# Performance work log

Hardware: AMD Instinct MI355X
Metric: run time of the kernel (lower is better)

The kernel has to match this reference:

```python
import jax, jax.numpy as jnp
import numpy as np

N_NODES = 100000
N_EDGES = 1000000
NUM_GRAPHS = 500
EPS = 1e-5


def gcn_conv(x, src, dst, W, b, n_nodes):
    # PyG GCNConv: h = x @ W, symmetric norm with self-loops, aggregate at dst, add bias
    h = x @ W
    deg = jnp.zeros((n_nodes,), h.dtype).at[dst].add(1.0) + 1.0  # in-degree + self-loop
    dis = jax.lax.rsqrt(deg)
    msg = h[src] * (dis[src] * dis[dst])[:, None]               # [E, F] gather
    agg = jnp.zeros_like(h).at[dst].add(msg)                    # scatter-add
    return agg + h * (dis * dis)[:, None] + b                   # self-loop term + bias


def bn_eval(x, g, be, m, v):
    return (x - m) * jax.lax.rsqrt(v + EPS) * g + be


def setup_inputs() -> dict:
    key = jax.random.key(0)
    ks = jax.random.split(key, 8)
    edge_index = jax.random.randint(ks[0], (2, N_EDGES), 0, N_NODES, dtype=jnp.int32)
    batch = jnp.sort(jax.random.randint(ks[1], (N_NODES,), 0, NUM_GRAPHS, dtype=jnp.int32))
    d_in, h1, h2, hc, nc = 64, 64, 32, 16, 2
    return {
        "x": jax.random.normal(ks[2], (N_NODES, d_in), jnp.float32),
        "edge_index": edge_index,
        "batch": batch,
        "W1": jax.random.normal(ks[3], (d_in, h1), jnp.float32) / np.sqrt(d_in),
        "b1": jnp.zeros((h1,), jnp.float32),
        "g1": jnp.ones((h1,), jnp.float32),
        "be1": jnp.zeros((h1,), jnp.float32),
        "m1": jnp.zeros((h1,), jnp.float32),
        "v1": jnp.ones((h1,), jnp.float32),
        "W2": jax.random.normal(ks[4], (h1, h2), jnp.float32) / np.sqrt(h1),
        "b2": jnp.zeros((h2,), jnp.float32),
        "g2": jnp.ones((h2,), jnp.float32),
        "be2": jnp.zeros((h2,), jnp.float32),
        "m2": jnp.zeros((h2,), jnp.float32),
        "v2": jnp.ones((h2,), jnp.float32),
        "Wc1": jax.random.normal(ks[5], (h2, hc), jnp.float32) / np.sqrt(h2),
        "bc1": jnp.zeros((hc,), jnp.float32),
        "Wc2": jax.random.normal(ks[6], (hc, nc), jnp.float32) / np.sqrt(hc),
        "bc2": jnp.zeros((nc,), jnp.float32),
    }


def reference(x, edge_index, batch, W1, b1, g1, be1, m1, v1,
              W2, b2, g2, be2, m2, v2, Wc1, bc1, Wc2, bc2):
    src, dst = edge_index[0], edge_index[1]
    n = x.shape[0]
    # encoder layer 1: GCNConv -> BN(eval) -> ReLU  (dropout off in eval)
    h = jax.nn.relu(bn_eval(gcn_conv(x, src, dst, W1, b1, n), g1, be1, m1, v1))
    # encoder layer 2
    h = jax.nn.relu(bn_eval(gcn_conv(h, src, dst, W2, b2, n), g2, be2, m2, v2))
    # global mean pool over graphs
    sums = jax.ops.segment_sum(h, batch, num_segments=NUM_GRAPHS)
    cnts = jax.ops.segment_sum(jnp.ones((n,), h.dtype), batch, num_segments=NUM_GRAPHS)
    z = sums / jnp.maximum(cnts, 1.0)[:, None]                  # [NUM_GRAPHS, h2]
    # classifier MLP
    return jax.nn.relu(z @ Wc1 + bc1) @ Wc2 + bc2               # [NUM_GRAPHS, num_classes]
```

## Files before the change

### kernel.cpp

```cpp
#include <hip/hip_runtime.h>
#include <hip/hip_bf16.h>


#define CHUNK 4096
#define CAP   4096

typedef float floatx2 __attribute__((ext_vector_type(2)));

__global__ void k_zero_misc(int* __restrict__ bucketCursor, float* __restrict__ sums,
                            int nSums) {
    int i = blockIdx.x * blockDim.x + threadIdx.x;
    if (i < 512) bucketCursor[i] = 0;
    int j = i - 512;
    if (j >= 0 && j < nSums) sums[j] = 0.f;
}

__global__ __launch_bounds__(256) void k_binpairs2(
    const int* __restrict__ src, const int* __restrict__ dst,
    int* __restrict__ bucketCursor, unsigned* __restrict__ pairs, int E) {
    __shared__ int lh[512];
    __shared__ int lbase[512];
    for (int i = threadIdx.x; i < 512; i += 256) lh[i] = 0;
    __syncthreads();
    int base = blockIdx.x * CHUNK;
    for (int i = threadIdx.x; i < CHUNK; i += 256) {
        int e = base + i;
        if (e < E) atomicAdd(&lh[dst[e] >> 8], 1);
    }
    __syncthreads();
    for (int i = threadIdx.x; i < 512; i += 256) {
        int c = lh[i];
        lbase[i] = c ? atomicAdd(&bucketCursor[i], c) : 0;
        lh[i] = 0;
    }
    __syncthreads();
    for (int i = threadIdx.x; i < CHUNK; i += 256) {
        int e = base + i;
        if (e < E) {
            int d = dst[e];
            int b = d >> 8;
            int r = atomicAdd(&lh[b], 1);
            pairs[(size_t)b * CAP + lbase[b] + r] =
                ((unsigned)src[e] << 8) | (unsigned)(d & 255);
        }
    }
}

__global__ __launch_bounds__(256) void k_csr2(
    const unsigned* __restrict__ pairs, const int* __restrict__ bucketCursor,
    int* __restrict__ rowStart, int* __restrict__ rowEnd,
    float* __restrict__ dis, int* __restrict__ perm, int n) {
    __shared__ int cnt[256];
    __shared__ int s[256];
    __shared__ int cur[256];
    int b = blockIdx.x, tid = threadIdx.x;
    int total = bucketCursor[b];
    size_t base = (size_t)b * CAP;
    cnt[tid] = 0;
    __syncthreads();
    for (int i = tid; i < total; i += 256) atomicAdd(&cnt[pairs[base + i] & 255], 1);
    __syncthreads();
    int v = cnt[tid];
    s[tid] = v;
    __syncthreads();
    for (int off = 1; off < 256; off <<= 1) {
        int t = (tid >= off) ? s[tid - off] : 0;
        __syncthreads();
        s[tid] += t;
        __syncthreads();
    }
    int excl = s[tid] - v;
    int node = b * 256 + tid;
    if (node < n) {
        rowStart[node] = (int)base + excl;
        rowEnd[node]   = (int)base + excl + v;
        dis[node] = rsqrtf((float)v + 1.0f);
    }
    cur[tid] = excl;
    __syncthreads();
    for (int i = tid; i < total; i += 256) {
        unsigned pr = pairs[base + i];
        int lo = pr & 255;
        int slot = atomicAdd(&cur[lo], 1);
        perm[base + slot] = (int)(pr >> 8);
    }
}

__global__ __launch_bounds__(256) void k_gemm64(
    const float* __restrict__ x, const float* __restrict__ W,
    const float* __restrict__ dis, unsigned char* __restrict__ hs8, int n) {
    __shared__ float Ws[64 * 64];
    __shared__ float xs[128][65];
    const int tid = threadIdx.x;
    for (int i = tid * 4; i < 4096; i += 1024)
        *(float4*)&Ws[i] = *(const float4*)&W[i];
    const int base = blockIdx.x * 128;
    for (int i = tid; i < 2048; i += 256) {
        int r = i >> 4;
        int k = (i & 15) * 4;
        int row = base + r;
        float4 xv = (row < n) ? *(const float4*)&x[(size_t)row * 64 + k]
                              : make_float4(0.f, 0.f, 0.f, 0.f);
        xs[r][k] = xv.x; xs[r][k + 1] = xv.y; xs[r][k + 2] = xv.z; xs[r][k + 3] = xv.w;
    }
    __syncthreads();
    const int cg = tid & 7;
    const int rg = tid >> 3;
    float acc[4][8] = {};
#pragma unroll 4
    for (int k = 0; k < 64; ++k) {
        float w8[8];
        *(float4*)&w8[0] = *(const float4*)&Ws[k * 64 + cg * 8];
        *(float4*)&w8[4] = *(const float4*)&Ws[k * 64 + cg * 8 + 4];
        float x4[4];
#pragma unroll
        for (int rr = 0; rr < 4; ++rr) x4[rr] = xs[rg * 4 + rr][k];
#pragma unroll
        for (int rr = 0; rr < 4; ++rr)
#pragma unroll
            for (int cc = 0; cc < 8; ++cc)
                acc[rr][cc] = fmaf(x4[rr], w8[cc], acc[rr][cc]);
    }
#pragma unroll
    for (int rr = 0; rr < 4; ++rr) {
        int row = base + rg * 4 + rr;
        if (row >= n) break;
        float d = dis[row];
        int q0 = __builtin_amdgcn_cvt_pk_fp8_f32(acc[rr][0] * d, acc[rr][1] * d, 0, false);
        q0 = __builtin_amdgcn_cvt_pk_fp8_f32(acc[rr][2] * d, acc[rr][3] * d, q0, true);
        int q1 = __builtin_amdgcn_cvt_pk_fp8_f32(acc[rr][4] * d, acc[rr][5] * d, 0, false);
        q1 = __builtin_amdgcn_cvt_pk_fp8_f32(acc[rr][6] * d, acc[rr][7] * d, q1, true);
        uint2 q = {(unsigned)q0, (unsigned)q1};
        *(uint2*)&hs8[(size_t)row * 64 + cg * 8] = q;
    }
}

__device__ __forceinline__ void unpack8(uint2 u, float* a) {
    floatx2 p0 = __builtin_amdgcn_cvt_pk_f32_fp8(u.x, false);
    floatx2 p1 = __builtin_amdgcn_cvt_pk_f32_fp8(u.x, true);
    floatx2 p2 = __builtin_amdgcn_cvt_pk_f32_fp8(u.y, false);
    floatx2 p3 = __builtin_amdgcn_cvt_pk_f32_fp8(u.y, true);
    a[0] = p0[0]; a[1] = p0[1]; a[2] = p1[0]; a[3] = p1[1];
    a[4] = p2[0]; a[5] = p2[1]; a[6] = p3[0]; a[7] = p3[1];
}

__global__ __launch_bounds__(256) void k_g64f8_gemm32(
    const unsigned char* __restrict__ hs8, const int* __restrict__ rowStart,
    const int* __restrict__ rowEnd, const int* __restrict__ perm,
    const float* __restrict__ dis,
    const float* __restrict__ b, const float* __restrict__ g,
    const float* __restrict__ be, const float* __restrict__ m,
    const float* __restrict__ v, const float* __restrict__ W2,
    unsigned char* __restrict__ hs2f8, int n) {
    __shared__ float W2s[64 * 32];
    __shared__ float actS[32][68];
    for (int i = threadIdx.x * 4; i < 2048; i += 1024)
        *(float4*)&W2s[i] = *(const float4*)&W2[i];
    __syncthreads();

    const uint2* hsu = (const uint2*)hs8;
    int c = threadIdx.x & 7;
    int ln = threadIdx.x >> 3;
    int node = (blockIdx.x * 256 + threadIdx.x) >> 3;
    if (node >= n) return;
    int r0 = rowStart[node], r1 = rowEnd[node];
    float d = dis[node];
    float a[8];
    unpack8(hsu[(size_t)node * 8 + c], a);
    int e = r0;
    for (; e + 7 < r1; e += 8) {
        int s0 = perm[e],     s1 = perm[e + 1], s2 = perm[e + 2], s3 = perm[e + 3];
        int s4 = perm[e + 4], s5 = perm[e + 5], s6 = perm[e + 6], s7 = perm[e + 7];
        uint2 u0 = hsu[(size_t)s0 * 8 + c];
        uint2 u1 = hsu[(size_t)s1 * 8 + c];
        uint2 u2 = hsu[(size_t)s2 * 8 + c];
        uint2 u3 = hsu[(size_t)s3 * 8 + c];
        uint2 u4 = hsu[(size_t)s4 * 8 + c];
        uint2 u5 = hsu[(size_t)s5 * 8 + c];
        uint2 u6 = hsu[(size_t)s6 * 8 + c];
        uint2 u7 = hsu[(size_t)s7 * 8 + c];
        float t[8];
#pragma unroll
        for (int j = 0; j < 8; ++j) {
            uint2 u = j == 0 ? u0 : j == 1 ? u1 : j == 2 ? u2 : j == 3 ? u3
                    : j == 4 ? u4 : j == 5 ? u5 : j == 6 ? u6 : u7;
            unpack8(u, t);
#pragma unroll
            for (int q = 0; q < 8; ++q) a[q] += t[q];
        }
    }
    for (; e < r1; ++e) {
        float t[8];
        unpack8(hsu[(size_t)perm[e] * 8 + c], t);
#pragma unroll
        for (int q = 0; q < 8; ++q) a[q] += t[q];
    }
    int f = 8 * c;
    float y[8];
#pragma unroll
    for (int h = 0; h < 2; ++h) {
        float4 gv = *(const float4*)&g[f + 4 * h];
        float4 vv = *(const float4*)&v[f + 4 * h];
        float4 bv = *(const float4*)&b[f + 4 * h];
        float4 mv = *(const float4*)&m[f + 4 * h];
        float4 bev = *(const float4*)&be[f + 4 * h];
        float sc0 = gv.x * rsqrtf(vv.x + 1e-5f), sc1 = gv.y * rsqrtf(vv.y + 1e-5f);
        float sc2 = gv.z * rsqrtf(vv.z + 1e-5f), sc3 = gv.w * rsqrtf(vv.w + 1e-5f);
        float y0 = fmaf(a[4 * h + 0] * d, sc0, (bv.x - mv.x) * sc0 + bev.x);
        float y1 = fmaf(a[4 * h + 1] * d, sc1, (bv.y - mv.y) * sc1 + bev.y);
        float y2 = fmaf(a[4 * h + 2] * d, sc2, (bv.z - mv.z) * sc2 + bev.z);
        float y3 = fmaf(a[4 * h + 3] * d, sc3, (bv.w - mv.w) * sc3 + bev.w);
        y[4 * h + 0] = y0 > 0.f ? y0 : 0.f;
        y[4 * h + 1] = y1 > 0.f ? y1 : 0.f;
        y[4 * h + 2] = y2 > 0.f ? y2 : 0.f;
        y[4 * h + 3] = y3 > 0.f ? y3 : 0.f;
    }
    *(float4*)&actS[ln][f]     = *(float4*)&y[0];
    *(float4*)&actS[ln][f + 4] = *(float4*)&y[4];

    float o0 = 0.f, o1 = 0.f, o2 = 0.f, o3 = 0.f;
#pragma unroll
    for (int k = 0; k < 64; ++k) {
        float av = actS[ln][k];
        float4 w = *(const float4*)&W2s[k * 32 + 4 * c];
        o0 = fmaf(av, w.x, o0);
        o1 = fmaf(av, w.y, o1);
        o2 = fmaf(av, w.z, o2);
        o3 = fmaf(av, w.w, o3);
    }
    int q = __builtin_amdgcn_cvt_pk_fp8_f32(o0 * d, o1 * d, 0, false);
    q = __builtin_amdgcn_cvt_pk_fp8_f32(o2 * d, o3 * d, q, true);
    *(unsigned*)&hs2f8[(size_t)node * 32 + 4 * c] = (unsigned)q;
}

__global__ __launch_bounds__(256) void k_g32f8(
    const unsigned char* __restrict__ hs8, const int* __restrict__ rowStart,
    const int* __restrict__ rowEnd, const int* __restrict__ perm,
    const float* __restrict__ dis,
    const float* __restrict__ b, const float* __restrict__ g,
    const float* __restrict__ be, const float* __restrict__ m,
    const float* __restrict__ v, float* __restrict__ act, int n) {
    const uint2* hsu = (const uint2*)hs8;
    int c = threadIdx.x & 3;
    int node = (blockIdx.x * 256 + threadIdx.x) >> 2;
    if (node >= n) return;
    int r0 = rowStart[node], r1 = rowEnd[node];
    float d = dis[node];
    float a[8];
    unpack8(hsu[(size_t)node * 4 + c], a);
    int e = r0;
    for (; e + 7 < r1; e += 8) {
        int s0 = perm[e],     s1 = perm[e + 1], s2 = perm[e + 2], s3 = perm[e + 3];
        int s4 = perm[e + 4], s5 = perm[e + 5], s6 = perm[e + 6], s7 = perm[e + 7];
        uint2 u0 = hsu[(size_t)s0 * 4 + c];
        uint2 u1 = hsu[(size_t)s1 * 4 + c];
        uint2 u2 = hsu[(size_t)s2 * 4 + c];
        uint2 u3 = hsu[(size_t)s3 * 4 + c];
        uint2 u4 = hsu[(size_t)s4 * 4 + c];
        uint2 u5 = hsu[(size_t)s5 * 4 + c];
        uint2 u6 = hsu[(size_t)s6 * 4 + c];
        uint2 u7 = hsu[(size_t)s7 * 4 + c];
        float t[8];
#pragma unroll
        for (int j = 0; j < 8; ++j) {
            uint2 u = j == 0 ? u0 : j == 1 ? u1 : j == 2 ? u2 : j == 3 ? u3
                    : j == 4 ? u4 : j == 5 ? u5 : j == 6 ? u6 : u7;
            unpack8(u, t);
#pragma unroll
            for (int q = 0; q < 8; ++q) a[q] += t[q];
        }
    }
    for (; e < r1; ++e) {
        float t[8];
        unpack8(hsu[(size_t)perm[e] * 4 + c], t);
#pragma unroll
        for (int q = 0; q < 8; ++q) a[q] += t[q];
    }
    int f = 8 * c;
#pragma unroll
    for (int h = 0; h < 2; ++h) {
        float4 gv = *(const float4*)&g[f + 4 * h];
        float4 vv = *(const float4*)&v[f + 4 * h];
        float4 bv = *(const float4*)&b[f + 4 * h];
        float4 mv = *(const float4*)&m[f + 4 * h];
        float4 bev = *(const float4*)&be[f + 4 * h];
        float sc0 = gv.x * rsqrtf(vv.x + 1e-5f), sc1 = gv.y * rsqrtf(vv.y + 1e-5f);
        float sc2 = gv.z * rsqrtf(vv.z + 1e-5f), sc3 = gv.w * rsqrtf(vv.w + 1e-5f);
        float y0 = fmaf(a[4 * h + 0] * d, sc0, (bv.x - mv.x) * sc0 + bev.x);
        float y1 = fmaf(a[4 * h + 1] * d, sc1, (bv.y - mv.y) * sc1 + bev.y);
        float y2 = fmaf(a[4 * h + 2] * d, sc2, (bv.z - mv.z) * sc2 + bev.z);
        float y3 = fmaf(a[4 * h + 3] * d, sc3, (bv.w - mv.w) * sc3 + bev.w);
        float4 o = {y0 > 0.f ? y0 : 0.f, y1 > 0.f ? y1 : 0.f,
                    y2 > 0.f ? y2 : 0.f, y3 > 0.f ? y3 : 0.f};
        *(float4*)&act[(size_t)node * 32 + f + 4 * h] = o;
    }
}

__global__ __launch_bounds__(256) void k_pool(
    const float* __restrict__ act2, const int* __restrict__ batch,
    float* __restrict__ sums, float* __restrict__ cnt, int n) {
    int f = threadIdx.x & 31;
    int chunk = (blockIdx.x * blockDim.x + threadIdx.x) >> 5;
    int nchunks = (gridDim.x * blockDim.x) >> 5;
    int per = (n + nchunks - 1) / nchunks;
    int i0 = chunk * per;
    int i1 = min(n, i0 + per);
    if (i0 >= n) return;
    float acc = 0.f, c = 0.f;
    int cur = batch[i0];
    for (int i = i0; i < i1; ++i) {
        int bg = batch[i];
        if (bg != cur) {
            atomicAdd(&sums[(size_t)cur * 32 + f], acc);
            if (f == 0) atomicAdd(&cnt[cur], c);
            acc = 0.f; c = 0.f; cur = bg;
        }
        acc += act2[(size_t)i * 32 + f];
        c += 1.f;
    }
    atomicAdd(&sums[(size_t)cur * 32 + f], acc);
    if (f == 0) atomicAdd(&cnt[cur], c);
}

__global__ void k_mlp(const float* __restrict__ sums, const float* __restrict__ cnt,
                      const float* __restrict__ Wc1, const float* __restrict__ bc1,
                      const float* __restrict__ Wc2, const float* __restrict__ bc2,
                      float* __restrict__ out, int G) {
    int g = blockIdx.x * blockDim.x + threadIdx.x;
    if (g >= G) return;
    float c = cnt[g];
    c = c < 1.f ? 1.f : c;
    float inv = 1.f / c;
    float z[32];
#pragma unroll
    for (int j = 0; j < 32; ++j) z[j] = sums[(size_t)g * 32 + j] * inv;
    float o0 = bc2[0], o1 = bc2[1];
#pragma unroll
    for (int k = 0; k < 16; ++k) {
        float t = bc1[k];
#pragma unroll
        for (int j = 0; j < 32; ++j) t = fmaf(z[j], Wc1[j * 16 + k], t);
        t = t > 0.f ? t : 0.f;
        o0 = fmaf(t, Wc2[k * 2 + 0], o0);
        o1 = fmaf(t, Wc2[k * 2 + 1], o1);
    }
    out[g * 2 + 0] = o0;
    out[g * 2 + 1] = o1;
}

extern "C" void kernel_launch(void* const* d_in, const int* in_sizes, int n_in,
                              void* d_out, int out_size, void* d_ws, size_t ws_size,
                              hipStream_t stream) {
    const float* x   = (const float*)d_in[0];
    const int* ei    = (const int*)d_in[1];
    const int* batch = (const int*)d_in[2];
    const float* W1  = (const float*)d_in[3];
    const float* b1  = (const float*)d_in[4];
    const float* g1  = (const float*)d_in[5];
    const float* be1 = (const float*)d_in[6];
    const float* m1  = (const float*)d_in[7];
    const float* v1  = (const float*)d_in[8];
    const float* W2  = (const float*)d_in[9];
    const float* b2  = (const float*)d_in[10];
    const float* g2  = (const float*)d_in[11];
    const float* be2 = (const float*)d_in[12];
    const float* m2  = (const float*)d_in[13];
    const float* v2  = (const float*)d_in[14];
    const float* Wc1 = (const float*)d_in[15];
    const float* bc1 = (const float*)d_in[16];
    const float* Wc2 = (const float*)d_in[17];
    const float* bc2 = (const float*)d_in[18];

    const int n = in_sizes[2];
    const int E = in_sizes[1] / 2;
    const int G = out_size / 2;
    const int* srcI = ei;
    const int* dstI = ei + E;
    const int NB = (n + 255) >> 8;

    char* pw = (char*)d_ws;
    auto alloc = [&](size_t bytes) {
        char* r = pw;
        pw += (bytes + 255) & ~(size_t)255;
        return r;
    };
    float*    dis          = (float*)alloc((size_t)n * 4);
    int*      bucketCursor = (int*)alloc(512 * 4);
    unsigned* pairs        = (unsigned*)alloc((size_t)NB * CAP * 4);
    int*      perm         = (int*)alloc((size_t)NB * CAP * 4);
    int*      rowStart     = (int*)alloc((size_t)n * 4);
    int*      rowEnd       = (int*)alloc((size_t)n * 4);
    unsigned char* hs1f8   = (unsigned char*)alloc((size_t)64 * n);
    unsigned char* hs2f8   = (unsigned char*)alloc((size_t)32 * n);
    float*    act2         = (float*)alloc((size_t)32 * n * 4);
    float*    sums         = (float*)alloc((size_t)32 * G * 4 + (size_t)G * 4);
    float*    cntG         = sums + (size_t)32 * G;

    const int NT = 256;
    const int nbE = (E + CHUNK - 1) / CHUNK;
    const int nSums = G * 33;

    k_zero_misc<<<(512 + nSums + NT - 1) / NT, NT, 0, stream>>>(bucketCursor, sums, nSums);
    k_binpairs2<<<nbE, NT, 0, stream>>>(srcI, dstI, bucketCursor, pairs, E);
    k_csr2<<<NB, NT, 0, stream>>>(pairs, bucketCursor, rowStart, rowEnd, dis, perm, n);

    k_gemm64<<<(n + 127) / 128, NT, 0, stream>>>(x, W1, dis, hs1f8, n);
    k_g64f8_gemm32<<<(n * 8 + NT - 1) / NT, NT, 0, stream>>>(
        hs1f8, rowStart, rowEnd, perm, dis, b1, g1, be1, m1, v1, W2, hs2f8, n);

    k_g32f8<<<(n * 4 + NT - 1) / NT, NT, 0, stream>>>(
        hs2f8, rowStart, rowEnd, perm, dis, b2, g2, be2, m2, v2, act2, n);

    k_pool<<<1024, NT, 0, stream>>>(act2, batch, sums, cntG, n);
    k_mlp<<<(G + NT - 1) / NT, NT, 0, stream>>>(sums, cntG, Wc1, bc1, Wc2, bc2,
                                                (float*)d_out, G);
}
```

Before: 128.0 us.

## Fuse layer-2 aggregation with global mean pooling via shared-memory atomics

Merges the second GCN aggregation kernel with the graph pooling kernel. Each block accumulates its nodes' post-ReLU features into per-graph shared-memory bins and then flushes them to global sums with atomics. This drops the full-size act2 intermediate write/read and one kernel launch. In exchange it adds contended LDS atomics, since most lanes in a block hit the same graph, plus extra global atomics per block.

```diff
diff --git a/kernel.cpp b/kernel.cpp
--- a/kernel.cpp
+++ b/kernel.cpp
@@ -233,93 +233,112 @@
     *(unsigned*)&hs2f8[(size_t)node * 32 + 4 * c] = (unsigned)q;
 }
 
-__global__ __launch_bounds__(256) void k_g32f8(
+__global__ __launch_bounds__(256) void k_g32f8_pool(
     const unsigned char* __restrict__ hs8, const int* __restrict__ rowStart,
     const int* __restrict__ rowEnd, const int* __restrict__ perm,
     const float* __restrict__ dis,
     const float* __restrict__ b, const float* __restrict__ g,
     const float* __restrict__ be, const float* __restrict__ m,
-    const float* __restrict__ v, float* __restrict__ act, int n) {
+    const float* __restrict__ v, const int* __restrict__ batch,
+    float* __restrict__ sums, float* __restrict__ cntG, int n) {
+    __shared__ float lsum[64][32];
+    __shared__ float lcnt[64];
     const uint2* hsu = (const uint2*)hs8;
-    int c = threadIdx.x & 3;
-    int node = (blockIdx.x * 256 + threadIdx.x) >> 2;
-    if (node >= n) return;
-    int r0 = rowStart[node], r1 = rowEnd[node];
-    float d = dis[node];
-    float a[8];
-    unpack8(hsu[(size_t)node * 4 + c], a);
-    int e = r0;
-    for (; e + 7 < r1; e += 8) {
-        int s0 = perm[e],     s1 = perm[e + 1], s2 = perm[e + 2], s3 = perm[e + 3];
-        int s4 = perm[e + 4], s5 = perm[e + 5], s6 = perm[e + 6], s7 = perm[e + 7];
-        uint2 u0 = hsu[(size_t)s0 * 4 + c];
-        uint2 u1 = hsu[(size_t)s1 * 4 + c];
-        uint2 u2 = hsu[(size_t)s2 * 4 + c];
-        uint2 u3 = hsu[(size_t)s3 * 4 + c];
-        uint2 u4 = hsu[(size_t)s4 * 4 + c];
-        uint2 u5 = hsu[(size_t)s5 * 4 + c];
-        uint2 u6 = hsu[(size_t)s6 * 4 + c];
-        uint2 u7 = hsu[(size_t)s7 * 4 + c];
-        float t[8];
-#pragma unroll
-        for (int j = 0; j < 8; ++j) {
-            uint2 u = j == 0 ? u0 : j == 1 ? u1 : j == 2 ? u2 : j == 3 ? u3
-                    : j == 4 ? u4 : j == 5 ? u5 : j == 6 ? u6 : u7;
-            unpack8(u, t);
+    int tid = threadIdx.x;
+    int c = tid & 3;
+    int node = (blockIdx.x * 256 + tid) >> 2;
+    int base = blockIdx.x * 64;
+    bool valid = node < n;
+
+    int lastNode = min(base + 63, n - 1);
+    int g0 = batch[base < n ? base : n - 1];
+    int span = batch[lastNode] - g0 + 1;
+    bool ldsPath = span <= 64;
+
+    if (ldsPath) {
+        for (int i = tid; i < span * 32; i += 256) lsum[i >> 5][i & 31] = 0.f;
+        for (int i = tid; i < span; i += 256) lcnt[i] = 0.f;
+    }
+    __syncthreads();
+
+    float y[8];
+    int f = 8 * c;
+    int bg = 0;
+    if (valid) {
+        int r0 = rowStart[node], r1 = rowEnd[node];
+        float d = dis[node];
+        float a[8];
+        unpack8(hsu[(size_t)node * 4 + c], a);
+        int e = r0;
+        for (; e + 7 < r1; e += 8) {
+            int s0 = perm[e],     s1 = perm[e + 1], s2 = perm[e + 2], s3 = perm[e + 3];
+            int s4 = perm[e + 4], s5 = perm[e + 5], s6 = perm[e + 6], s7 = perm[e + 7];
+            uint2 u0 = hsu[(size_t)s0 * 4 + c];
+            uint2 u1 = hsu[(size_t)s1 * 4 + c];
+            uint2 u2 = hsu[(size_t)s2 * 4 + c];
+            uint2 u3 = hsu[(size_t)s3 * 4 + c];
+            uint2 u4 = hsu[(size_t)s4 * 4 + c];
+            uint2 u5 = hsu[(size_t)s5 * 4 + c];
+            uint2 u6 = hsu[(size_t)s6 * 4 + c];
+            uint2 u7 = hsu[(size_t)s7 * 4 + c];
+            float t[8];
+#pragma unroll
+            for (int j = 0; j < 8; ++j) {
+                uint2 u = j == 0 ? u0 : j == 1 ? u1 : j == 2 ? u2 : j == 3 ? u3
+                        : j == 4 ? u4 : j == 5 ? u5 : j == 6 ? u6 : u7;
+                unpack8(u, t);
+#pragma unroll
+                for (int q = 0; q < 8; ++q) a[q] += t[q];
+            }
+        }
+        for (; e < r1; ++e) {
+            float t[8];
+            unpack8(hsu[(size_t)perm[e] * 4 + c], t);
 #pragma unroll
             for (int q = 0; q < 8; ++q) a[q] += t[q];
         }
-    }
-    for (; e < r1; ++e) {
-        float t[8];
-        unpack8(hsu[(size_t)perm[e] * 4 + c], t);
-#pragma unroll
-        for (int q = 0; q < 8; ++q) a[q] += t[q];
-    }
-    int f = 8 * c;
-#pragma unroll
-    for (int h = 0; h < 2; ++h) {
-        float4 gv = *(const float4*)&g[f + 4 * h];
-        float4 vv = *(const float4*)&v[f + 4 * h];
-        float4 bv = *(const float4*)&b[f + 4 * h];
-        float4 mv = *(const float4*)&m[f + 4 * h];
-        float4 bev = *(const float4*)&be[f + 4 * h];
-        float sc0 = gv.x * rsqrtf(vv.x + 1e-5f), sc1 = gv.y * rsqrtf(vv.y + 1e-5f);
-        float sc2 = gv.z * rsqrtf(vv.z + 1e-5f), sc3 = gv.w * rsqrtf(vv.w + 1e-5f);
-        float y0 = fmaf(a[4 * h + 0] * d, sc0, (bv.x - mv.x) * sc0 + bev.x);
-        float y1 = fmaf(a[4 * h + 1] * d, sc1, (bv.y - mv.y) * sc1 + bev.y);
-        float y2 = fmaf(a[4 * h + 2] * d, sc2, (bv.z - mv.z) * sc2 + bev.z);
-        float y3 = fmaf(a[4 * h + 3] * d, sc3, (bv.w - mv.w) * sc3 + bev.w);
-        float4 o = {y0 > 0.f ? y0 : 0.f, y1 > 0.f ? y1 : 0.f,
-                    y2 > 0.f ? y2 : 0.f, y3 > 0.f ? y3 : 0.f};
-        *(float4*)&act[(size_t)node * 32 + f + 4 * h] = o;
-    }
-}
-
-__global__ __launch_bounds__(256) void k_pool(
-    const float* __restrict__ act2, const int* __restrict__ batch,
-    float* __restrict__ sums, float* __restrict__ cnt, int n) {
-    int f = threadIdx.x & 31;
-    int chunk = (blockIdx.x * blockDim.x + threadIdx.x) >> 5;
-    int nchunks = (gridDim.x * blockDim.x) >> 5;
-    int per = (n + nchunks - 1) / nchunks;
-    int i0 = chunk * per;
-    int i1 = min(n, i0 + per);
-    if (i0 >= n) return;
-    float acc = 0.f, c = 0.f;
-    int cur = batch[i0];
-    for (int i = i0; i < i1; ++i) {
-        int bg = batch[i];
-        if (bg != cur) {
-            atomicAdd(&sums[(size_t)cur * 32 + f], acc);
-            if (f == 0) atomicAdd(&cnt[cur], c);
-            acc = 0.f; c = 0.f; cur = bg;
-        }
-        acc += act2[(size_t)i * 32 + f];
-        c += 1.f;
-    }
-    atomicAdd(&sums[(size_t)cur * 32 + f], acc);
-    if (f == 0) atomicAdd(&cnt[cur], c);
+#pragma unroll
+        for (int h = 0; h < 2; ++h) {
+            float4 gv = *(const float4*)&g[f + 4 * h];
+            float4 vv = *(const float4*)&v[f + 4 * h];
+            float4 bv = *(const float4*)&b[f + 4 * h];
+            float4 mv = *(const float4*)&m[f + 4 * h];
+            float4 bev = *(const float4*)&be[f + 4 * h];
+            float sc0 = gv.x * rsqrtf(vv.x + 1e-5f), sc1 = gv.y * rsqrtf(vv.y + 1e-5f);
+            float sc2 = gv.z * rsqrtf(vv.z + 1e-5f), sc3 = gv.w * rsqrtf(vv.w + 1e-5f);
+            float y0 = fmaf(a[4 * h + 0] * d, sc0, (bv.x - mv.x) * sc0 + bev.x);
+            float y1 = fmaf(a[4 * h + 1] * d, sc1, (bv.y - mv.y) * sc1 + bev.y);
+            float y2 = fmaf(a[4 * h + 2] * d, sc2, (bv.z - mv.z) * sc2 + bev.z);
+            float y3 = fmaf(a[4 * h + 3] * d, sc3, (bv.w - mv.w) * sc3 + bev.w);
+            y[4 * h + 0] = y0 > 0.f ? y0 : 0.f;
+            y[4 * h + 1] = y1 > 0.f ? y1 : 0.f;
+            y[4 * h + 2] = y2 > 0.f ? y2 : 0.f;
+            y[4 * h + 3] = y3 > 0.f ? y3 : 0.f;
+        }
+        bg = batch[node];
+        if (ldsPath) {
+            int gl = bg - g0;
+#pragma unroll
+            for (int j = 0; j < 8; ++j) atomicAdd(&lsum[gl][f + j], y[j]);
+            if (c == 0) atomicAdd(&lcnt[gl], 1.f);
+        } else {
+#pragma unroll
+            for (int j = 0; j < 8; ++j) atomicAdd(&sums[(size_t)bg * 32 + f + j], y[j]);
+            if (c == 0) atomicAdd(&cntG[bg], 1.f);
+        }
+    }
+    __syncthreads();
+    if (ldsPath) {
+        for (int i = tid; i < span * 32; i += 256) {
+            int gs = i >> 5, ff = i & 31;
+            float vl = lsum[gs][ff];
+            if (vl != 0.f) atomicAdd(&sums[(size_t)(g0 + gs) * 32 + ff], vl);
+        }
+        for (int i = tid; i < span; i += 256) {
+            float vl = lcnt[i];
+            if (vl != 0.f) atomicAdd(&cntG[g0 + i], vl);
+        }
+    }
 }
 
 __global__ void k_mlp(const float* __restrict__ sums, const float* __restrict__ cnt,
@@ -392,7 +411,6 @@
     int*      rowEnd       = (int*)alloc((size_t)n * 4);
     unsigned char* hs1f8   = (unsigned char*)alloc((size_t)64 * n);
     unsigned char* hs2f8   = (unsigned char*)alloc((size_t)32 * n);
-    float*    act2         = (float*)alloc((size_t)32 * n * 4);
     float*    sums         = (float*)alloc((size_t)32 * G * 4 + (size_t)G * 4);
     float*    cntG         = sums + (size_t)32 * G;
 
@@ -408,10 +426,10 @@
     k_g64f8_gemm32<<<(n * 8 + NT - 1) / NT, NT, 0, stream>>>(
         hs1f8, rowStart, rowEnd, perm, dis, b1, g1, be1, m1, v1, W2, hs2f8, n);
 
-    k_g32f8<<<(n * 4 + NT - 1) / NT, NT, 0, stream>>>(
-        hs2f8, rowStart, rowEnd, perm, dis, b2, g2, be2, m2, v2, act2, n);
-
-    k_pool<<<1024, NT, 0, stream>>>(act2, batch, sums, cntG, n);
+    k_g32f8_pool<<<(n * 4 + NT - 1) / NT, NT, 0, stream>>>(
+        hs2f8, rowStart, rowEnd, perm, dis, b2, g2, be2, m2, v2, batch,
+        sums, cntG, n);
+
     k_mlp<<<(G + NT - 1) / NT, NT, 0, stream>>>(sums, cntG, Wc1, bc1, Wc2, bc2,
                                                 (float*)d_out, G);
 }
```

Measured after the change: 128.0 us. No clear change (-0.0%).
